# Performance work log

Hardware: AMD Instinct MI355X
Metric: run time of the kernel (lower is better)

Reference implementation:

```python
import jax, jax.numpy as jnp
import numpy as np

N, L, D = 256, 512, 512


def _attention(x, W_in, W_out, apply_tanh):
    # x: [N, L, D]; 'general' attention: project query, score against context (=x)
    q = jnp.einsum('bld,ed->ble', x, W_in)          # [N, L, D]
    scores = jnp.einsum('bld,bmd->blm', q, x)       # [N, L, L]
    w = jax.nn.softmax(scores, axis=-1)             # softmax over keys
    mix = jnp.einsum('blm,bmd->bld', w, x)          # [N, L, D]
    comb = jnp.concatenate([mix, q], axis=-1)       # [N, L, 2D]
    out = jnp.einsum('blc,dc->bld', comb, W_out)    # Linear(2D, D), no bias
    return jnp.tanh(out) if apply_tanh else out


def setup_inputs() -> dict:
    key = jax.random.key(0)
    k1, k2, k3, k4, k5 = jax.random.split(key, 5)
    s = 0.02
    return {
        'embeddings': jax.random.normal(k1, (N, L, D), dtype=jnp.float32),
        'W_in1': jax.random.normal(k2, (D, D), dtype=jnp.float32) * s,
        'W_out1': jax.random.normal(k3, (D, 2 * D), dtype=jnp.float32) * s,
        'W_in2': jax.random.normal(k4, (D, D), dtype=jnp.float32) * s,
        'W_out2': jax.random.normal(k5, (D, 2 * D), dtype=jnp.float32) * s,
    }


def reference(embeddings, W_in1, W_out1, W_in2, W_out2):
    x = _attention(embeddings, W_in1, W_out1, apply_tanh=True)   # block 1 (tanh)
    x = _attention(x, W_in2, W_out2, apply_tanh=False)           # block 2 (no tanh)
    # transpose(1,2) + avg_pool1d over full length == mean over L
    pooled = jnp.mean(x, axis=1)                                  # [N, D]
    return pooled.reshape(pooled.shape[0], -1, 1, 1)              # [N, D, 1, 1]
```

## Files before the change

### kernel.cpp

```cpp
#include <hip/hip_runtime.h>
#include <cstdint>
#include <cstddef>

typedef uint16_t u16;
typedef __attribute__((ext_vector_type(8))) short bf16x8;
typedef __attribute__((ext_vector_type(4))) float f32x4;
typedef __attribute__((ext_vector_type(4))) uint16_t u16x4;

#define GLOBAL_AS(p) (const __attribute__((address_space(1))) void*)(p)
#define LDS_AS(p)    (__attribute__((address_space(3))) void*)(p)

__device__ __forceinline__ void bar_vm4(){
  asm volatile("s_waitcnt vmcnt(4)" ::: "memory");
  __builtin_amdgcn_s_barrier();
  asm volatile("" ::: "memory");
}
__device__ __forceinline__ void bar_vm0(){
  asm volatile("s_waitcnt vmcnt(0)" ::: "memory");
  __builtin_amdgcn_s_barrier();
  asm volatile("" ::: "memory");
}
__device__ __forceinline__ void bar_end(){
  asm volatile("" ::: "memory");
  __builtin_amdgcn_s_barrier();
  asm volatile("" ::: "memory");
}
__device__ __forceinline__ void bar_lgkm(){
  asm volatile("s_waitcnt lgkmcnt(0)" ::: "memory");
  __builtin_amdgcn_s_barrier();
  asm volatile("" ::: "memory");
}

__device__ __forceinline__ u16 f2b(float f){
  uint32_t u = __float_as_uint(f);
  u += 0x7fff + ((u >> 16) & 1);
  return (u16)(u >> 16);
}

__global__ void cvt_bf16_kernel(const float* __restrict__ src, u16* __restrict__ dst, int n){
  int i = (blockIdx.x * 256 + threadIdx.x) * 4;
  if (i >= n) return;
  float4 f = *(const float4*)(src + i);
  u16x4 o; o.x = f2b(f.x); o.y = f2b(f.y); o.z = f2b(f.z); o.w = f2b(f.w);
  *(u16x4*)(dst + i) = o;
}

__global__ void cvtT_kernel(const float* __restrict__ src, u16* __restrict__ x, u16* __restrict__ xT){
  __shared__ u16 tile[64][68];
  size_t b = blockIdx.y;
  int t = blockIdx.x;
  int r0 = (t >> 3) * 64, c0 = (t & 7) * 64;
  const float* s = src + b * 262144;
  u16* dx = x + b * 262144;
  u16* dT = xT + b * 262144;
  int tx = threadIdx.x & 63, ty = threadIdx.x >> 6;
  #pragma unroll
  for (int k = 0; k < 16; k++){
    int r = ty * 16 + k;
    u16 v = f2b(s[(size_t)(r0 + r) * 512 + c0 + tx]);
    dx[(size_t)(r0 + r) * 512 + c0 + tx] = v;
    tile[r][tx] = v;
  }
  __syncthreads();
  #pragma unroll
  for (int k = 0; k < 16; k++){
    int c = ty * 16 + k;
    dT[(size_t)(c0 + c) * 512 + r0 + tx] = tile[tx][c];
  }
}

__global__ void transpose512_kernel(const u16* __restrict__ src, u16* __restrict__ dst){
  __shared__ u16 tile[64][68];
  size_t b = blockIdx.y;
  int t = blockIdx.x;
  int r0 = (t >> 3) * 64, c0 = (t & 7) * 64;
  const u16* s = src + b * 262144;
  u16* d = dst + b * 262144;
  int tx = threadIdx.x & 63, ty = threadIdx.x >> 6;
  #pragma unroll
  for (int k = 0; k < 16; k++){
    int r = ty * 16 + k;
    tile[r][tx] = s[(size_t)(r0 + r) * 512 + c0 + tx];
  }
  __syncthreads();
  #pragma unroll
  for (int k = 0; k < 16; k++){
    int c = ty * 16 + k;
    d[(size_t)(c0 + c) * 512 + r0 + tx] = tile[tx][c];
  }
}

__global__ __launch_bounds__(512, 2) void attn_kernel(
    const u16* __restrict__ q, const u16* __restrict__ x, const u16* __restrict__ xT,
    u16* __restrict__ mix, int batPerXcd)
{
  __shared__ __align__(16) u16 U[64 * 520];
  __shared__ __align__(16) u16 Bx[2][8][64 * 32];
  __shared__ float stats[2][64][8];
  const int64_t E = 262144;
  int id = blockIdx.x;
  int tile = (id >> 3) & 7;
  int64_t bat = (int64_t)(id & 7) * batPerXcd + (id >> 6);
  q += bat * E; x += bat * E; xT += bat * E; mix += bat * E;
  int m0 = tile * 64;
  int tid = threadIdx.x, lane = tid & 63, w = tid >> 6;
  int fr = lane & 15, qd = lane >> 4;
  int fq = qd * 8;
  int bslot = (qd ^ ((fr >> 1) & 3)) * 8;

  auto stage = [&](const u16* __restrict__ src, int buf, int k0){
    #pragma unroll
    for (int s = 0; s < 4; s++){
      int rloc = s * 16 + (lane >> 2);
      int chunk = (lane & 3) ^ ((rloc >> 1) & 3);
      const u16* g = src + (size_t)(w * 64 + rloc) * 512 + k0 + chunk * 8;
      __builtin_amdgcn_global_load_lds(GLOBAL_AS(g), LDS_AS(&Bx[buf][w][s * 512 + lane * 8]), 16, 0, 0);
    }
  };

  #pragma unroll
  for (int c = 0; c < 8; c++){
    int row = c * 8 + w;
    __builtin_amdgcn_global_load_lds(GLOBAL_AS(q + (size_t)(m0 + row) * 512 + lane * 8),
                                     LDS_AS(&U[row * 520 + lane * 8]), 16, 0, 0);
  }
  stage(x, 0, 0);
  stage(x, 1, 32);
  asm volatile("s_waitcnt vmcnt(8)" ::: "memory");
  __builtin_amdgcn_s_barrier();
  asm volatile("" ::: "memory");

  f32x4 acc[4][4];
  #pragma unroll
  for (int i = 0; i < 4; i++)
    #pragma unroll
    for (int j = 0; j < 4; j++) acc[i][j] = (f32x4){0.f, 0.f, 0.f, 0.f};

  #pragma unroll
  for (int it = 0; it < 16; ++it){
    asm volatile("s_waitcnt vmcnt(4)" ::: "memory");
    int k0 = it * 32;
    bf16x8 af[4], bfr[4];
    #pragma unroll
    for (int i = 0; i < 4; i++) af[i]  = *(const bf16x8*)&U[(i * 16 + fr) * 520 + k0 + fq];
    #pragma unroll
    for (int j = 0; j < 4; j++) bfr[j] = *(const bf16x8*)&Bx[it & 1][w][(j * 16 + fr) * 32 + bslot];
    asm volatile("s_waitcnt lgkmcnt(0)" ::: "memory");
    if (it <= 13)      stage(x,  it & 1, (it + 2) * 32);
    else if (it == 14) stage(xT, 0, 0);
    else               stage(xT, 1, 32);
    #pragma unroll
    for (int i = 0; i < 4; i++)
      #pragma unroll
      for (int j = 0; j < 4; j++)
        acc[i][j] = __builtin_amdgcn_mfma_f32_16x16x32_bf16(af[i], bfr[j], acc[i][j], 0, 0, 0);
  }

  float inv[4][4];
  #pragma unroll
  for (int i = 0; i < 4; i++)
    #pragma unroll
    for (int r = 0; r < 4; r++){
      float m = acc[i][0][r];
      #pragma unroll
      for (int j = 1; j < 4; j++) m = fmaxf(m, acc[i][j][r]);
      #pragma unroll
      for (int o = 1; o <= 8; o <<= 1) m = fmaxf(m, __shfl_xor(m, o));
      if (fr == 0) stats[0][i * 16 + qd * 4 + r][w] = m;
    }
  bar_lgkm();
  #pragma unroll
  for (int i = 0; i < 4; i++)
    #pragma unroll
    for (int r = 0; r < 4; r++){
      int row = i * 16 + qd * 4 + r;
      float m = stats[0][row][0];
      #pragma unroll
      for (int t = 1; t < 8; t++) m = fmaxf(m, stats[0][row][t]);
      float s = 0.f;
      #pragma unroll
      for (int j = 0; j < 4; j++){
        float e = __expf(acc[i][j][r] - m);
        acc[i][j][r] = e; s += e;
      }
      #pragma unroll
      for (int o = 1; o <= 8; o <<= 1) s += __shfl_xor(s, o);
      if (fr == 0) stats[1][row][w] = s;
    }
  bar_lgkm();
  #pragma unroll
  for (int i = 0; i < 4; i++)
    #pragma unroll
    for (int r = 0; r < 4; r++){
      int row = i * 16 + qd * 4 + r;
      float s = stats[1][row][0];
      #pragma unroll
      for (int t = 1; t < 8; t++) s += stats[1][row][t];
      inv[i][r] = 1.0f / s;
    }
  #pragma unroll
  for (int i = 0; i < 4; i++)
    #pragma unroll
    for (int r = 0; r < 4; r++)
      #pragma unroll
      for (int j = 0; j < 4; j++){
        int row = i * 16 + qd * 4 + r;
        int col = w * 64 + j * 16 + fr;
        uint32_t mine = f2b(acc[i][j][r] * inv[i][r]);
        uint32_t oth = (uint32_t)__shfl_xor((int)mine, 1);
        if (!(fr & 1)) *(uint32_t*)&U[row * 520 + col] = mine | (oth << 16);
      }
  bar_lgkm();

  #pragma unroll
  for (int i = 0; i < 4; i++)
    #pragma unroll
    for (int j = 0; j < 4; j++) acc[i][j] = (f32x4){0.f, 0.f, 0.f, 0.f};
  #pragma unroll
  for (int it = 0; it < 16; ++it){
    if (it < 15) asm volatile("s_waitcnt vmcnt(4)" ::: "memory");
    else         asm volatile("s_waitcnt vmcnt(0)" ::: "memory");
    int k0 = it * 32;
    bf16x8 af[4], bfr[4];
    #pragma unroll
    for (int i = 0; i < 4; i++) af[i]  = *(const bf16x8*)&U[(i * 16 + fr) * 520 + k0 + fq];
    #pragma unroll
    for (int j = 0; j < 4; j++) bfr[j] = *(const bf16x8*)&Bx[it & 1][w][(j * 16 + fr) * 32 + bslot];
    asm volatile("s_waitcnt lgkmcnt(0)" ::: "memory");
    if (it <= 13) stage(xT, it & 1, (it + 2) * 32);
    #pragma unroll
    for (int i = 0; i < 4; i++)
      #pragma unroll
      for (int j = 0; j < 4; j++)
        acc[i][j] = __builtin_amdgcn_mfma_f32_16x16x32_bf16(af[i], bfr[j], acc[i][j], 0, 0, 0);
  }
  #pragma unroll
  for (int i = 0; i < 4; i++)
    #pragma unroll
    for (int j = 0; j < 4; j++)
      #pragma unroll
      for (int r = 0; r < 4; r++)
        mix[(size_t)(m0 + i * 16 + qd * 4 + r) * 512 + w * 64 + j * 16 + fr] =
            f2b(acc[i][j][r]);
}

template<bool SPLIT, bool TANH, bool POOL, typename CT>
__global__ __launch_bounds__(256, 2) void gemm_bt_kernel(
    const u16* __restrict__ A0, const u16* __restrict__ A1,
    const u16* __restrict__ B, CT* __restrict__ C,
    int K, int ldb, int64_t aBatch, int64_t bBatch, int64_t cBatch,
    float* __restrict__ poolOut, int b0)
{
  __shared__ __align__(16) u16 As[2][128 * 32];
  __shared__ __align__(16) u16 Bs[2][128 * 32];
  int64_t bat = blockIdx.y;
  int m0 = (blockIdx.x & 3) * 128, n0 = (blockIdx.x >> 2) * 128;
  A0 += bat * aBatch;
  if (SPLIT) A1 += bat * aBatch;
  B += bat * bBatch;
  if (!POOL) C += bat * cBatch;
  int tid = threadIdx.x, lane = tid & 63;
  int w = tid >> 6;
  int wm = (w >> 1) * 64, wn = (w & 1) * 64;
  f32x4 acc[4][4];
  #pragma unroll
  for (int i = 0; i < 4; i++)
    #pragma unroll
    for (int j = 0; j < 4; j++) acc[i][j] = (f32x4){0.f, 0.f, 0.f, 0.f};

  int sRow = tid >> 2;
  int sCol = ((tid & 3) ^ ((tid >> 3) & 3)) * 8;
  int fr = lane & 15;
  int fq = ((lane >> 4) ^ ((fr >> 1) & 3)) * 8;

  auto stageG = [&](int buf, int k0){
    const u16* Ap = A0; int kk = k0;
    if (SPLIT && k0 >= 512){ Ap = A1; kk = k0 - 512; }
    const u16* ga = Ap + (size_t)(m0 + sRow) * 512 + kk + sCol;
    const u16* gb = B  + (size_t)(n0 + sRow) * ldb + k0 + sCol;
    __builtin_amdgcn_global_load_lds(GLOBAL_AS(ga),                    LDS_AS(&As[buf][tid * 8]),        16, 0, 0);
    __builtin_amdgcn_global_load_lds(GLOBAL_AS(ga + (size_t)64 * 512), LDS_AS(&As[buf][2048 + tid * 8]), 16, 0, 0);
    __builtin_amdgcn_global_load_lds(GLOBAL_AS(gb),                    LDS_AS(&Bs[buf][tid * 8]),        16, 0, 0);
    __builtin_amdgcn_global_load_lds(GLOBAL_AS(gb + (size_t)64 * ldb), LDS_AS(&Bs[buf][2048 + tid * 8]), 16, 0, 0);
  };

  stageG(0, 0);

  int nIt = K >> 5;
  for (int it = 0; it < nIt; ++it){
    if (it + 1 < nIt){ stageG((it + 1) & 1, (it + 1) * 32); bar_vm4(); }
    else             { bar_vm0(); }
    bf16x8 af[4], bfr[4];
    #pragma unroll
    for (int i = 0; i < 4; i++) af[i]  = *(const bf16x8*)&As[it & 1][(wm + i * 16 + fr) * 32 + fq];
    #pragma unroll
    for (int j = 0; j < 4; j++) bfr[j] = *(const bf16x8*)&Bs[it & 1][(wn + j * 16 + fr) * 32 + fq];
    #pragma unroll
    for (int i = 0; i < 4; i++)
      #pragma unroll
      for (int j = 0; j < 4; j++)
        acc[i][j] = __builtin_amdgcn_mfma_f32_16x16x32_bf16(af[i], bfr[j], acc[i][j], 0, 0, 0);
    bar_end();
  }

  if constexpr (POOL){
    #pragma unroll
    for (int j = 0; j < 4; j++){
      float p = 0.f;
      #pragma unroll
      for (int i = 0; i < 4; i++)
        #pragma unroll
        for (int r = 0; r < 4; r++) p += acc[i][j][r];
      p += __shfl_xor(p, 16);
      p += __shfl_xor(p, 32);
      if (lane < 16){
        int col = n0 + wn + j * 16 + lane;
        atomicAdd(poolOut + ((size_t)(b0) + bat) * 512 + col, p * (1.0f / 512.0f));
      }
    }
  } else {
    int cq = (lane >> 4) * 4, cc = lane & 15;
    #pragma unroll
    for (int i = 0; i < 4; i++){
      #pragma unroll
      for (int j = 0; j < 4; j++){
        #pragma unroll
        for (int r = 0; r < 4; r++){
          int row = m0 + wm + i * 16 + cq + r;
          int col = n0 + wn + j * 16 + cc;
          float v = acc[i][j][r];
          if (TANH) v = tanhf(v);
          if constexpr (sizeof(CT) == 4) C[(size_t)row * 512 + col] = v;
          else                           C[(size_t)row * 512 + col] = f2b(v);
        }
      }
    }
  }
}

extern "C" void kernel_launch(void* const* d_in, const int* in_sizes, int n_in,
                              void* d_out, int out_size, void* d_ws, size_t ws_size,
                              hipStream_t stream) {
  const float* emb   = (const float*)d_in[0];
  const float* Win1  = (const float*)d_in[1];
  const float* Wout1 = (const float*)d_in[2];
  const float* Win2  = (const float*)d_in[3];
  const float* Wout2 = (const float*)d_in[4];
  float* out = (float*)d_out;

  int CB = 256;
  while (CB > 8 && (4ull << 20) + (size_t)CB * (5ull * 524288ull) > ws_size) CB >>= 1;
  const int64_t E = 262144;

  char* wsb = (char*)d_ws;
  u16* Win1b  = (u16*)wsb;
  u16* Wout1b = Win1b + 262144;
  u16* Win2b  = Wout1b + 524288;
  u16* Wout2b = Win2b + 262144;
  u16* base = (u16*)(wsb + (4 << 20));
  u16* Ar = base;
  u16* Br = base + (size_t)CB * E;
  u16* Cr = base + 2 * (size_t)CB * E;
  u16* Dr = base + 3 * (size_t)CB * E;
  u16* Fr = base + 4 * (size_t)CB * E;

  hipMemsetAsync(d_out, 0, (size_t)out_size * sizeof(float), stream);

  cvt_bf16_kernel<<<256, 256, 0, stream>>>(Win1,  Win1b,  262144);
  cvt_bf16_kernel<<<512, 256, 0, stream>>>(Wout1, Wout1b, 524288);
  cvt_bf16_kernel<<<256, 256, 0, stream>>>(Win2,  Win2b,  262144);
  cvt_bf16_kernel<<<512, 256, 0, stream>>>(Wout2, Wout2b, 524288);

  dim3 gg(16, CB);
  dim3 gt(64, CB);
  int nAttnBlocks = CB * 8;
  int batPerXcd = CB / 8;

  for (int c = 0; c < 256 / CB; c++){
    const float* embc = emb + (size_t)c * CB * 262144;
    int b0 = c * CB;

    cvtT_kernel<<<gt, 256, 0, stream>>>(embc, Ar, Cr);
    gemm_bt_kernel<false,false,false,u16><<<gg, 256, 0, stream>>>(
        Ar, nullptr, Win1b, Br, 512, 512, E, 0, E, nullptr, 0);
    attn_kernel<<<nAttnBlocks, 512, 0, stream>>>(Br, Ar, Cr, Fr, batPerXcd);
    gemm_bt_kernel<true,true,false,u16><<<gg, 256, 0, stream>>>(
        Fr, Br, Wout1b, Dr, 1024, 1024, E, 0, E, nullptr, 0);

    transpose512_kernel<<<gt, 256, 0, stream>>>(Dr, Cr);
    gemm_bt_kernel<false,false,false,u16><<<gg, 256, 0, stream>>>(
        Dr, nullptr, Win2b, Ar, 512, 512, E, 0, E, nullptr, 0);
    attn_kernel<<<nAttnBlocks, 512, 0, stream>>>(Ar, Dr, Cr, Fr, batPerXcd);
    gemm_bt_kernel<true,false,true,u16><<<gg, 256, 0, stream>>>(
        Fr, Ar, Wout2b, (u16*)nullptr, 1024, 1024, E, 0, 0, out, b0);
  }
}
```

Before: 1.632 ms.

## Remap GEMM and transpose blocks per XCD, drop GEMM double buffering and swizzle

```diff
diff --git a/kernel.cpp b/kernel.cpp
--- a/kernel.cpp
+++ b/kernel.cpp
@@ -10,21 +10,6 @@
 #define GLOBAL_AS(p) (const __attribute__((address_space(1))) void*)(p)
 #define LDS_AS(p)    (__attribute__((address_space(3))) void*)(p)
 
-__device__ __forceinline__ void bar_vm4(){
-  asm volatile("s_waitcnt vmcnt(4)" ::: "memory");
-  __builtin_amdgcn_s_barrier();
-  asm volatile("" ::: "memory");
-}
-__device__ __forceinline__ void bar_vm0(){
-  asm volatile("s_waitcnt vmcnt(0)" ::: "memory");
-  __builtin_amdgcn_s_barrier();
-  asm volatile("" ::: "memory");
-}
-__device__ __forceinline__ void bar_end(){
-  asm volatile("" ::: "memory");
-  __builtin_amdgcn_s_barrier();
-  asm volatile("" ::: "memory");
-}
 __device__ __forceinline__ void bar_lgkm(){
   asm volatile("s_waitcnt lgkmcnt(0)" ::: "memory");
   __builtin_amdgcn_s_barrier();
@@ -45,10 +30,13 @@
   *(u16x4*)(dst + i) = o;
 }
 
-__global__ void cvtT_kernel(const float* __restrict__ src, u16* __restrict__ x, u16* __restrict__ xT){
+__global__ void cvtT_kernel(const float* __restrict__ src, u16* __restrict__ x,
+                            u16* __restrict__ xT, int batPerXcd){
   __shared__ u16 tile[64][68];
-  size_t b = blockIdx.y;
-  int t = blockIdx.x;
+  int bid = blockIdx.x;
+  int xcd = bid & 7, serial = bid >> 3;
+  size_t b = (size_t)xcd * batPerXcd + (serial >> 6);
+  int t = serial & 63;
   int r0 = (t >> 3) * 64, c0 = (t & 7) * 64;
   const float* s = src + b * 262144;
   u16* dx = x + b * 262144;
@@ -69,10 +57,13 @@
   }
 }
 
-__global__ void transpose512_kernel(const u16* __restrict__ src, u16* __restrict__ dst){
+__global__ void transpose512_kernel(const u16* __restrict__ src, u16* __restrict__ dst,
+                                    int batPerXcd){
   __shared__ u16 tile[64][68];
-  size_t b = blockIdx.y;
-  int t = blockIdx.x;
+  int bid = blockIdx.x;
+  int xcd = bid & 7, serial = bid >> 3;
+  size_t b = (size_t)xcd * batPerXcd + (serial >> 6);
+  int t = serial & 63;
   int r0 = (t >> 3) * 64, c0 = (t & 7) * 64;
   const u16* s = src + b * 262144;
   u16* d = dst + b * 262144;
@@ -249,12 +240,15 @@
     const u16* __restrict__ A0, const u16* __restrict__ A1,
     const u16* __restrict__ B, CT* __restrict__ C,
     int K, int ldb, int64_t aBatch, int64_t bBatch, int64_t cBatch,
-    float* __restrict__ poolOut, int b0)
+    float* __restrict__ poolOut, int b0, int batPerXcd)
 {
-  __shared__ __align__(16) u16 As[2][128 * 32];
-  __shared__ __align__(16) u16 Bs[2][128 * 32];
-  int64_t bat = blockIdx.y;
-  int m0 = (blockIdx.x & 3) * 128, n0 = (blockIdx.x >> 2) * 128;
+  __shared__ __align__(16) u16 As[128 * 32];
+  __shared__ __align__(16) u16 Bs[128 * 32];
+  int bid = blockIdx.x;
+  int xcd = bid & 7, serial = bid >> 3;
+  int64_t bat = (int64_t)xcd * batPerXcd + (serial >> 4);
+  int bx = serial & 15;
+  int m0 = (bx & 3) * 128, n0 = (bx >> 2) * 128;
   A0 += bat * aBatch;
   if (SPLIT) A1 += bat * aBatch;
   B += bat * bBatch;
@@ -268,39 +262,30 @@
     #pragma unroll
     for (int j = 0; j < 4; j++) acc[i][j] = (f32x4){0.f, 0.f, 0.f, 0.f};
 
-  int sRow = tid >> 2;
-  int sCol = ((tid & 3) ^ ((tid >> 3) & 3)) * 8;
-  int fr = lane & 15;
-  int fq = ((lane >> 4) ^ ((fr >> 1) & 3)) * 8;
-
-  auto stageG = [&](int buf, int k0){
+  int sRow = tid >> 2, sCol = (tid & 3) * 8;
+  int fr = lane & 15, fq = (lane >> 4) * 8;
+
+  for (int k0 = 0; k0 < K; k0 += 32){
     const u16* Ap = A0; int kk = k0;
     if (SPLIT && k0 >= 512){ Ap = A1; kk = k0 - 512; }
     const u16* ga = Ap + (size_t)(m0 + sRow) * 512 + kk + sCol;
     const u16* gb = B  + (size_t)(n0 + sRow) * ldb + k0 + sCol;
-    __builtin_amdgcn_global_load_lds(GLOBAL_AS(ga),                    LDS_AS(&As[buf][tid * 8]),        16, 0, 0);
-    __builtin_amdgcn_global_load_lds(GLOBAL_AS(ga + (size_t)64 * 512), LDS_AS(&As[buf][2048 + tid * 8]), 16, 0, 0);
-    __builtin_amdgcn_global_load_lds(GLOBAL_AS(gb),                    LDS_AS(&Bs[buf][tid * 8]),        16, 0, 0);
-    __builtin_amdgcn_global_load_lds(GLOBAL_AS(gb + (size_t)64 * ldb), LDS_AS(&Bs[buf][2048 + tid * 8]), 16, 0, 0);
-  };
-
-  stageG(0, 0);
-
-  int nIt = K >> 5;
-  for (int it = 0; it < nIt; ++it){
-    if (it + 1 < nIt){ stageG((it + 1) & 1, (it + 1) * 32); bar_vm4(); }
-    else             { bar_vm0(); }
+    __builtin_amdgcn_global_load_lds(GLOBAL_AS(ga),                    LDS_AS(&As[tid * 8]),        16, 0, 0);
+    __builtin_amdgcn_global_load_lds(GLOBAL_AS(ga + (size_t)64 * 512), LDS_AS(&As[2048 + tid * 8]), 16, 0, 0);
+    __builtin_amdgcn_global_load_lds(GLOBAL_AS(gb),                    LDS_AS(&Bs[tid * 8]),        16, 0, 0);
+    __builtin_amdgcn_global_load_lds(GLOBAL_AS(gb + (size_t)64 * ldb), LDS_AS(&Bs[2048 + tid * 8]), 16, 0, 0);
+    __syncthreads();
     bf16x8 af[4], bfr[4];
     #pragma unroll
-    for (int i = 0; i < 4; i++) af[i]  = *(const bf16x8*)&As[it & 1][(wm + i * 16 + fr) * 32 + fq];
-    #pragma unroll
-    for (int j = 0; j < 4; j++) bfr[j] = *(const bf16x8*)&Bs[it & 1][(wn + j * 16 + fr) * 32 + fq];
+    for (int i = 0; i < 4; i++) af[i]  = *(const bf16x8*)&As[(wm + i * 16 + fr) * 32 + fq];
+    #pragma unroll
+    for (int j = 0; j < 4; j++) bfr[j] = *(const bf16x8*)&Bs[(wn + j * 16 + fr) * 32 + fq];
     #pragma unroll
     for (int i = 0; i < 4; i++)
       #pragma unroll
       for (int j = 0; j < 4; j++)
         acc[i][j] = __builtin_amdgcn_mfma_f32_16x16x32_bf16(af[i], bfr[j], acc[i][j], 0, 0, 0);
-    bar_end();
+    __syncthreads();
   }
 
   if constexpr (POOL){
@@ -371,8 +356,8 @@
   cvt_bf16_kernel<<<256, 256, 0, stream>>>(Win2,  Win2b,  262144);
   cvt_bf16_kernel<<<512, 256, 0, stream>>>(Wout2, Wout2b, 524288);
 
-  dim3 gg(16, CB);
-  dim3 gt(64, CB);
+  int nGemmBlocks = CB * 16;
+  int nTileBlocks = CB * 64;
   int nAttnBlocks = CB * 8;
   int batPerXcd = CB / 8;
 
@@ -380,18 +365,18 @@
     const float* embc = emb + (size_t)c * CB * 262144;
     int b0 = c * CB;
 
-    cvtT_kernel<<<gt, 256, 0, stream>>>(embc, Ar, Cr);
-    gemm_bt_kernel<false,false,false,u16><<<gg, 256, 0, stream>>>(
-        Ar, nullptr, Win1b, Br, 512, 512, E, 0, E, nullptr, 0);
+    cvtT_kernel<<<nTileBlocks, 256, 0, stream>>>(embc, Ar, Cr, batPerXcd);
+    gemm_bt_kernel<false,false,false,u16><<<nGemmBlocks, 256, 0, stream>>>(
+        Ar, nullptr, Win1b, Br, 512, 512, E, 0, E, nullptr, 0, batPerXcd);
     attn_kernel<<<nAttnBlocks, 512, 0, stream>>>(Br, Ar, Cr, Fr, batPerXcd);
-    gemm_bt_kernel<true,true,false,u16><<<gg, 256, 0, stream>>>(
-        Fr, Br, Wout1b, Dr, 1024, 1024, E, 0, E, nullptr, 0);
-
-    transpose512_kernel<<<gt, 256, 0, stream>>>(Dr, Cr);
-    gemm_bt_kernel<false,false,false,u16><<<gg, 256, 0, stream>>>(
-        Dr, nullptr, Win2b, Ar, 512, 512, E, 0, E, nullptr, 0);
+    gemm_bt_kernel<true,true,false,u16><<<nGemmBlocks, 256, 0, stream>>>(
+        Fr, Br, Wout1b, Dr, 1024, 1024, E, 0, E, nullptr, 0, batPerXcd);
+
+    transpose512_kernel<<<nTileBlocks, 256, 0, stream>>>(Dr, Cr, batPerXcd);
+    gemm_bt_kernel<false,false,false,u16><<<nGemmBlocks, 256, 0, stream>>>(
+        Dr, nullptr, Win2b, Ar, 512, 512, E, 0, E, nullptr, 0, batPerXcd);
     attn_kernel<<<nAttnBlocks, 512, 0, stream>>>(Ar, Dr, Cr, Fr, batPerXcd);
-    gemm_bt_kernel<true,false,true,u16><<<gg, 256, 0, stream>>>(
-        Fr, Ar, Wout2b, (u16*)nullptr, 1024, 1024, E, 0, 0, out, b0);
-  }
-}
+    gemm_bt_kernel<true,false,true,u16><<<nGemmBlocks, 256, 0, stream>>>(
+        Fr, Ar, Wout2b, (u16*)nullptr, 1024, 1024, E, 0, 0, out, b0, batPerXcd);
+  }
+}
```

After: 1.635 ms. Within noise of the previous version (+0.2%).
